# Kernel tuning notes

Measured on AMD Instinct MI355X. Metric: run time of the kernel, lower is better.

The kernel has to match this reference:

```python
import jax, jax.numpy as jnp
import numpy as np

HIDDEN = 3072
INTER = 8192
B, S = 4, 2048


def setup_inputs() -> dict:
    key = jax.random.key(0)
    k1, k2, k3, k4, k5 = jax.random.split(key, 5)
    hidden_states = jax.random.normal(k1, (B, S, HIDDEN), dtype=jnp.float32)
    # int8-valued quantized weights (stored as int32), per-output-channel scales
    gate_up_w_q = jax.random.randint(k2, (2 * INTER, HIDDEN), -128, 128, dtype=jnp.int32)
    gate_up_scale = jax.random.uniform(k3, (2 * INTER,), dtype=jnp.float32) * 0.01
    down_w_q = jax.random.randint(k4, (HIDDEN, INTER), -128, 128, dtype=jnp.int32)
    down_scale = jax.random.uniform(k5, (HIDDEN,), dtype=jnp.float32) * 0.01
    return {
        "hidden_states": hidden_states,
        "gate_up_w_q": gate_up_w_q,
        "gate_up_scale": gate_up_scale,
        "down_w_q": down_w_q,
        "down_scale": down_scale,
    }


def reference(hidden_states, gate_up_w_q, gate_up_scale, down_w_q, down_scale):
    # Inline dequant: W = W_q * scale (per output channel)
    w_gu = gate_up_w_q.astype(jnp.float32) * gate_up_scale[:, None]   # [2I, H]
    up_states = jnp.einsum("bsh,oh->bso", hidden_states, w_gu)        # [B, S, 2I]
    gate, up = jnp.split(up_states, 2, axis=-1)                       # each [B, S, I]
    h = up * jax.nn.silu(gate)                                        # SwiGLU
    w_d = down_w_q.astype(jnp.float32) * down_scale[:, None]          # [H, I]
    return jnp.einsum("bsi,hi->bsh", h, w_d)                          # [B, S, H]
```

## Files before the change

### kernel.cpp

```cpp
#include <hip/hip_runtime.h>
#include <hip/hip_bf16.h>

#define HIDDEN 3072
#define INTER  8192
#define NTOK   8192

typedef __attribute__((ext_vector_type(8))) short bf16x8;
typedef __attribute__((ext_vector_type(4))) float f32x4;

__device__ __forceinline__ void gload_lds16(const void* g, void* l) {
  __builtin_amdgcn_global_load_lds(
      (const __attribute__((address_space(1))) void*)g,
      (__attribute__((address_space(3))) void*)l, 16, 0, 0);
}

__device__ __forceinline__ unsigned short f2bf(float f) {
  unsigned int u = __builtin_bit_cast(unsigned int, f);
  u += 0x7fffu + ((u >> 16) & 1u);
  return (unsigned short)(u >> 16);
}


__global__ void cvt_f32_bf16(const float* __restrict__ in,
                             unsigned short* __restrict__ out, int n4) {
  int i = blockIdx.x * blockDim.x + threadIdx.x;
  if (i >= n4) return;
  float4 v = reinterpret_cast<const float4*>(in)[i];
  ushort4 o;
  o.x = f2bf(v.x); o.y = f2bf(v.y); o.z = f2bf(v.z); o.w = f2bf(v.w);
  reinterpret_cast<ushort4*>(out)[i] = o;
}

__global__ void cvt_i32_bf16(const int* __restrict__ in,
                             unsigned short* __restrict__ out, int n4) {
  int i = blockIdx.x * blockDim.x + threadIdx.x;
  if (i >= n4) return;
  int4 v = reinterpret_cast<const int4*>(in)[i];
  ushort4 o;
  o.x = f2bf((float)v.x); o.y = f2bf((float)v.y);
  o.z = f2bf((float)v.z); o.w = f2bf((float)v.w);
  reinterpret_cast<ushort4*>(out)[i] = o;
}

__global__ void cvt_wgu_perm(const int* __restrict__ in,
                             unsigned short* __restrict__ out) {
  int i4 = blockIdx.x * blockDim.x + threadIdx.x;
  const int RW = HIDDEN / 4;
  if (i4 >= 2 * INTER * RW) return;
  int rowp = i4 / RW;
  int col4 = i4 - rowp * RW;
  int c = ((rowp >> 5) << 4) + (rowp & 15);
  int u = (rowp >> 4) & 1;
  int srow = u * INTER + c;
  int4 v = reinterpret_cast<const int4*>(in)[(size_t)srow * RW + col4];
  ushort4 o;
  o.x = f2bf((float)v.x); o.y = f2bf((float)v.y);
  o.z = f2bf((float)v.z); o.w = f2bf((float)v.w);
  reinterpret_cast<ushort4*>(out)[i4] = o;
}


template<int K, int N, bool SWIGLU>
__global__ __launch_bounds__(512, 2) void gemm8p(
    const unsigned short* __restrict__ A,
    const unsigned short* __restrict__ B,
    const float* __restrict__ scale,
    void* __restrict__ outv)
{
  constexpr int NT = K / 64;
  __shared__ __align__(16) unsigned short lds[2][2][2][256 * 32];

  const int nbn = N / 256;
  const int nwg = (NTOK / 256) * nbn;
  int bid = blockIdx.x;
  int wg = (bid & 7) * (nwg >> 3) + (bid >> 3);
  const int bm = (wg / nbn) * 256;
  const int bn = (wg % nbn) * 256;

  const int tid  = threadIdx.x;
  const int lane = tid & 63;
  const int wid  = tid >> 6;
  const int wr = wid >> 2;
  const int wc = wid & 3;

  const int srow0 = tid >> 2;
  const int srow1 = 128 + (tid >> 2);
  const int scb   = tid & 3;

  const unsigned short* Ab = A + (size_t)bm * K;
  const unsigned short* Bb = B + (size_t)bn * K;

  auto stage = [&](const unsigned short* Gb, int op, int tt, int kh) {
    if (tt >= NT) return;
    int p = tt & 1;
    int kc = tt * 64 + kh * 32;
    unsigned short* lbase = &lds[p][op][kh][0];
    gload_lds16(Gb + (size_t)srow0 * K + kc + ((scb ^ ((srow0 >> 1) & 3)) * 8),
                lbase + (size_t)tid * 8);
    gload_lds16(Gb + (size_t)srow1 * K + kc + ((scb ^ ((srow1 >> 1) & 3)) * 8),
                lbase + (size_t)(512 + tid) * 8);
  };

  auto readA = [&](int p, int kh, int m) -> bf16x8 {
    int row = wr * 128 + m * 16 + (lane & 15);
    int cb = (lane >> 4) ^ ((row >> 1) & 3);
    return *(const bf16x8*)&lds[p][0][kh][row * 32 + cb * 8];
  };
  auto readB = [&](int p, int kh, int n) -> bf16x8 {
    int row = wc * 64 + n * 16 + (lane & 15);
    int cb = (lane >> 4) ^ ((row >> 1) & 3);
    return *(const bf16x8*)&lds[p][1][kh][row * 32 + cb * 8];
  };

  f32x4 acc[8][4] = {};
  bf16x8 af[8];

  stage(Ab, 0, 0, 0);
  stage(Bb, 1, 0, 0);
  stage(Ab, 0, 0, 1);
  stage(Bb, 1, 0, 1);
  stage(Ab, 0, 1, 0);
  stage(Bb, 1, 1, 0);
  stage(Ab, 0, 1, 1);
  asm volatile("s_waitcnt vmcnt(10)" ::: "memory");
  __builtin_amdgcn_s_barrier();

  for (int t = 0; t < NT; ++t) {
    const int pr = t & 1;
#pragma unroll
    for (int m = 0; m < 8; ++m) af[m] = readA(pr, 0, m);
    bf16x8 b0 = readB(pr, 0, 0);
    bf16x8 b1 = readB(pr, 0, 1);
    stage(Bb, 1, t + 1, 1);
    __builtin_amdgcn_s_barrier();
    __builtin_amdgcn_s_setprio(1);
#pragma unroll
    for (int m = 0; m < 8; ++m) {
      acc[m][0] = __builtin_amdgcn_mfma_f32_16x16x32_bf16(af[m], b0, acc[m][0], 0, 0, 0);
      acc[m][1] = __builtin_amdgcn_mfma_f32_16x16x32_bf16(af[m], b1, acc[m][1], 0, 0, 0);
    }
    __builtin_amdgcn_s_setprio(0);
    __builtin_amdgcn_s_barrier();

    b0 = readB(pr, 0, 2);
    b1 = readB(pr, 0, 3);
    stage(Ab, 0, t + 2, 0);
    __builtin_amdgcn_s_barrier();
    __builtin_amdgcn_s_setprio(1);
#pragma unroll
    for (int m = 0; m < 8; ++m) {
      acc[m][2] = __builtin_amdgcn_mfma_f32_16x16x32_bf16(af[m], b0, acc[m][2], 0, 0, 0);
      acc[m][3] = __builtin_amdgcn_mfma_f32_16x16x32_bf16(af[m], b1, acc[m][3], 0, 0, 0);
    }
    __builtin_amdgcn_s_setprio(0);
    if (t + 2 < NT) {
      asm volatile("s_waitcnt vmcnt(10)" ::: "memory");
    } else if (t + 1 < NT) {
      asm volatile("s_waitcnt vmcnt(8)" ::: "memory");
    } else {
      asm volatile("s_waitcnt vmcnt(0)" ::: "memory");
    }
    __builtin_amdgcn_s_barrier();

#pragma unroll
    for (int m = 0; m < 8; ++m) af[m] = readA(pr, 1, m);
    b0 = readB(pr, 1, 0);
    b1 = readB(pr, 1, 1);
    stage(Bb, 1, t + 2, 0);
    __builtin_amdgcn_s_barrier();
    __builtin_amdgcn_s_setprio(1);
#pragma unroll
    for (int m = 0; m < 8; ++m) {
      acc[m][0] = __builtin_amdgcn_mfma_f32_16x16x32_bf16(af[m], b0, acc[m][0], 0, 0, 0);
      acc[m][1] = __builtin_amdgcn_mfma_f32_16x16x32_bf16(af[m], b1, acc[m][1], 0, 0, 0);
    }
    __builtin_amdgcn_s_setprio(0);
    __builtin_amdgcn_s_barrier();

    b0 = readB(pr, 1, 2);
    b1 = readB(pr, 1, 3);
    stage(Ab, 0, t + 2, 1);
    __builtin_amdgcn_s_barrier();
    __builtin_amdgcn_s_setprio(1);
#pragma unroll
    for (int m = 0; m < 8; ++m) {
      acc[m][2] = __builtin_amdgcn_mfma_f32_16x16x32_bf16(af[m], b0, acc[m][2], 0, 0, 0);
      acc[m][3] = __builtin_amdgcn_mfma_f32_16x16x32_bf16(af[m], b1, acc[m][3], 0, 0, 0);
    }
    __builtin_amdgcn_s_setprio(0);
    if (t + 2 < NT) {
      asm volatile("s_waitcnt vmcnt(10)" ::: "memory");
    } else if (t + 1 < NT) {
      asm volatile("s_waitcnt vmcnt(4)" ::: "memory");
    } else {
      asm volatile("s_waitcnt vmcnt(0)" ::: "memory");
    }
    __builtin_amdgcn_s_barrier();
  }

  const int crow0 = (lane >> 4) * 4;
  const int ccol  = lane & 15;
  if constexpr (SWIGLU) {
    unsigned short* H = (unsigned short*)outv;
    const int hbase = (bn >> 1) + wc * 32;
#pragma unroll
    for (int np = 0; np < 2; ++np) {
      int hcol = hbase + np * 16 + ccol;
      float sg = scale[hcol];
      float su = scale[INTER + hcol];
#pragma unroll
      for (int m = 0; m < 8; ++m) {
#pragma unroll
        for (int j = 0; j < 4; ++j) {
          int row = bm + wr * 128 + m * 16 + crow0 + j;
          float g = acc[m][2 * np + 0][j] * sg;
          float u = acc[m][2 * np + 1][j] * su;
          float s = g / (1.0f + __expf(-g));
          H[(size_t)row * INTER + hcol] = f2bf(u * s);
        }
      }
    }
  } else {
    float* O = (float*)outv;
#pragma unroll
    for (int n = 0; n < 4; ++n) {
      int col = bn + wc * 64 + n * 16 + ccol;
      float sc = scale[col];
#pragma unroll
      for (int m = 0; m < 8; ++m) {
#pragma unroll
        for (int j = 0; j < 4; ++j) {
          int row = bm + wr * 128 + m * 16 + crow0 + j;
          O[(size_t)row * N + col] = acc[m][n][j] * sc;
        }
      }
    }
  }
}


extern "C" void kernel_launch(void* const* d_in, const int* in_sizes, int n_in,
                              void* d_out, int out_size, void* d_ws, size_t ws_size,
                              hipStream_t stream) {
  (void)in_sizes; (void)n_in; (void)out_size; (void)ws_size;

  const float* hidden = (const float*)d_in[0];
  const int*   guq    = (const int*)d_in[1];
  const float* gus    = (const float*)d_in[2];
  const int*   dwq    = (const int*)d_in[3];
  const float* dsc    = (const float*)d_in[4];
  float* out = (float*)d_out;

  char* ws = (char*)d_ws;
  unsigned short* xb  = (unsigned short*)(ws);
  unsigned short* wgu = (unsigned short*)(ws + 50331648ull);
  unsigned short* wd  = (unsigned short*)(ws + 150994944ull);
  unsigned short* hb  = (unsigned short*)(ws + 201326592ull);

  {
    int n4 = NTOK * HIDDEN / 4;
    cvt_f32_bf16<<<(n4 + 255) / 256, 256, 0, stream>>>(hidden, xb, n4);
  }
  {
    int n4 = 2 * INTER * HIDDEN / 4;
    cvt_wgu_perm<<<(n4 + 255) / 256, 256, 0, stream>>>(guq, wgu);
  }
  {
    int n4 = HIDDEN * INTER / 4;
    cvt_i32_bf16<<<(n4 + 255) / 256, 256, 0, stream>>>(dwq, wd, n4);
  }

  gemm8p<HIDDEN, 2 * INTER, true>
      <<<(NTOK / 256) * (2 * INTER / 256), 512, 0, stream>>>(xb, wgu, gus, hb);
  gemm8p<INTER, HIDDEN, false>
      <<<(NTOK / 256) * (HIDDEN / 256), 512, 0, stream>>>(hb, wd, dsc, out);
}
```

Before: 1.267 ms.

## Switch to 32x32x16 MFMA tiles and split-K the down GEMM

Both GEMMs move from 16x16x32 to 32x32x16 bf16 MFMA instructions. Per-wave register fragments and LDS reads are reorganised to match, and the gate/up weight permutation now interleaves in 32-row groups so the SwiGLU epilogue still pairs gate and up columns. The down-projection GEMM is split along K into two slices to double the workgroup count and fill the CUs better. Partial results are combined with float atomicAdd into an output that a new kernel zeroes first, which adds extra atomic traffic and makes the summation order nondeterministic.

```diff
diff --git a/kernel.cpp b/kernel.cpp
--- a/kernel.cpp
+++ b/kernel.cpp
@@ -6,7 +6,7 @@
 #define NTOK   8192
 
 typedef __attribute__((ext_vector_type(8))) short bf16x8;
-typedef __attribute__((ext_vector_type(4))) float f32x4;
+typedef __attribute__((ext_vector_type(16))) float f32x16;
 
 __device__ __forceinline__ void gload_lds16(const void* g, void* l) {
   __builtin_amdgcn_global_load_lds(
@@ -49,9 +49,9 @@
   if (i4 >= 2 * INTER * RW) return;
   int rowp = i4 / RW;
   int col4 = i4 - rowp * RW;
-  int c = ((rowp >> 5) << 4) + (rowp & 15);
-  int u = (rowp >> 4) & 1;
-  int srow = u * INTER + c;
+  int h = ((rowp >> 6) << 5) + (rowp & 31);
+  int u = (rowp >> 5) & 1;
+  int srow = u * INTER + h;
   int4 v = reinterpret_cast<const int4*>(in)[(size_t)srow * RW + col4];
   ushort4 o;
   o.x = f2bf((float)v.x); o.y = f2bf((float)v.y);
@@ -59,23 +59,33 @@
   reinterpret_cast<ushort4*>(out)[i4] = o;
 }
 
-
-template<int K, int N, bool SWIGLU>
+__global__ void zero_out(float* __restrict__ out, int n4) {
+  int stride = gridDim.x * blockDim.x;
+  for (int i = blockIdx.x * blockDim.x + threadIdx.x; i < n4; i += stride)
+    reinterpret_cast<float4*>(out)[i] = make_float4(0.f, 0.f, 0.f, 0.f);
+}
+
+
+template<int STRIDE, int KLEN, int N, int KSPLIT, int MODE>
 __global__ __launch_bounds__(512, 2) void gemm8p(
     const unsigned short* __restrict__ A,
     const unsigned short* __restrict__ B,
     const float* __restrict__ scale,
     void* __restrict__ outv)
 {
-  constexpr int NT = K / 64;
+  constexpr int NT = KLEN / 64;
   __shared__ __align__(16) unsigned short lds[2][2][2][256 * 32];
 
   const int nbn = N / 256;
-  const int nwg = (NTOK / 256) * nbn;
+  const int ntmn = (NTOK / 256) * nbn;
+  const int nwg = ntmn * KSPLIT;
   int bid = blockIdx.x;
   int wg = (bid & 7) * (nwg >> 3) + (bid >> 3);
-  const int bm = (wg / nbn) * 256;
-  const int bn = (wg % nbn) * 256;
+  const int kslice = wg / ntmn;
+  const int local = wg - kslice * ntmn;
+  const int bm = (local / nbn) * 256;
+  const int bn = (local % nbn) * 256;
+  const int koff = kslice * KLEN;
 
   const int tid  = threadIdx.x;
   const int lane = tid & 63;
@@ -87,33 +97,34 @@
   const int srow1 = 128 + (tid >> 2);
   const int scb   = tid & 3;
 
-  const unsigned short* Ab = A + (size_t)bm * K;
-  const unsigned short* Bb = B + (size_t)bn * K;
+  const unsigned short* Ab = A + (size_t)bm * STRIDE + koff;
+  const unsigned short* Bb = B + (size_t)bn * STRIDE + koff;
 
   auto stage = [&](const unsigned short* Gb, int op, int tt, int kh) {
     if (tt >= NT) return;
     int p = tt & 1;
     int kc = tt * 64 + kh * 32;
     unsigned short* lbase = &lds[p][op][kh][0];
-    gload_lds16(Gb + (size_t)srow0 * K + kc + ((scb ^ ((srow0 >> 1) & 3)) * 8),
+    gload_lds16(Gb + (size_t)srow0 * STRIDE + kc + ((scb ^ ((srow0 >> 1) & 3)) * 8),
                 lbase + (size_t)tid * 8);
-    gload_lds16(Gb + (size_t)srow1 * K + kc + ((scb ^ ((srow1 >> 1) & 3)) * 8),
+    gload_lds16(Gb + (size_t)srow1 * STRIDE + kc + ((scb ^ ((srow1 >> 1) & 3)) * 8),
                 lbase + (size_t)(512 + tid) * 8);
   };
 
-  auto readA = [&](int p, int kh, int m) -> bf16x8 {
-    int row = wr * 128 + m * 16 + (lane & 15);
-    int cb = (lane >> 4) ^ ((row >> 1) & 3);
+  auto readA = [&](int p, int kh, int m, int ks) -> bf16x8 {
+    int row = wr * 128 + m * 32 + (lane & 31);
+    int cb = (ks * 2 + (lane >> 5)) ^ ((row >> 1) & 3);
     return *(const bf16x8*)&lds[p][0][kh][row * 32 + cb * 8];
   };
-  auto readB = [&](int p, int kh, int n) -> bf16x8 {
-    int row = wc * 64 + n * 16 + (lane & 15);
-    int cb = (lane >> 4) ^ ((row >> 1) & 3);
+  auto readB = [&](int p, int kh, int n, int ks) -> bf16x8 {
+    int row = wc * 64 + n * 32 + (lane & 31);
+    int cb = (ks * 2 + (lane >> 5)) ^ ((row >> 1) & 3);
     return *(const bf16x8*)&lds[p][1][kh][row * 32 + cb * 8];
   };
 
-  f32x4 acc[8][4] = {};
-  bf16x8 af[8];
+  f32x16 acc[4][2] = {};
+  bf16x8 af[4][2];
+  bf16x8 b0, b1;
 
   stage(Ab, 0, 0, 0);
   stage(Bb, 1, 0, 0);
@@ -128,29 +139,32 @@
   for (int t = 0; t < NT; ++t) {
     const int pr = t & 1;
 #pragma unroll
-    for (int m = 0; m < 8; ++m) af[m] = readA(pr, 0, m);
-    bf16x8 b0 = readB(pr, 0, 0);
-    bf16x8 b1 = readB(pr, 0, 1);
+    for (int m = 0; m < 4; ++m) {
+      af[m][0] = readA(pr, 0, m, 0);
+      af[m][1] = readA(pr, 0, m, 1);
+    }
+    b0 = readB(pr, 0, 0, 0);
+    b1 = readB(pr, 0, 0, 1);
     stage(Bb, 1, t + 1, 1);
     __builtin_amdgcn_s_barrier();
     __builtin_amdgcn_s_setprio(1);
 #pragma unroll
-    for (int m = 0; m < 8; ++m) {
-      acc[m][0] = __builtin_amdgcn_mfma_f32_16x16x32_bf16(af[m], b0, acc[m][0], 0, 0, 0);
-      acc[m][1] = __builtin_amdgcn_mfma_f32_16x16x32_bf16(af[m], b1, acc[m][1], 0, 0, 0);
-    }
-    __builtin_amdgcn_s_setprio(0);
-    __builtin_amdgcn_s_barrier();
-
-    b0 = readB(pr, 0, 2);
-    b1 = readB(pr, 0, 3);
+    for (int m = 0; m < 4; ++m) {
+      acc[m][0] = __builtin_amdgcn_mfma_f32_32x32x16_bf16(af[m][0], b0, acc[m][0], 0, 0, 0);
+      acc[m][0] = __builtin_amdgcn_mfma_f32_32x32x16_bf16(af[m][1], b1, acc[m][0], 0, 0, 0);
+    }
+    __builtin_amdgcn_s_setprio(0);
+    __builtin_amdgcn_s_barrier();
+
+    b0 = readB(pr, 0, 1, 0);
+    b1 = readB(pr, 0, 1, 1);
     stage(Ab, 0, t + 2, 0);
     __builtin_amdgcn_s_barrier();
     __builtin_amdgcn_s_setprio(1);
 #pragma unroll
-    for (int m = 0; m < 8; ++m) {
-      acc[m][2] = __builtin_amdgcn_mfma_f32_16x16x32_bf16(af[m], b0, acc[m][2], 0, 0, 0);
-      acc[m][3] = __builtin_amdgcn_mfma_f32_16x16x32_bf16(af[m], b1, acc[m][3], 0, 0, 0);
+    for (int m = 0; m < 4; ++m) {
+      acc[m][1] = __builtin_amdgcn_mfma_f32_32x32x16_bf16(af[m][0], b0, acc[m][1], 0, 0, 0);
+      acc[m][1] = __builtin_amdgcn_mfma_f32_32x32x16_bf16(af[m][1], b1, acc[m][1], 0, 0, 0);
     }
     __builtin_amdgcn_s_setprio(0);
     if (t + 2 < NT) {
@@ -163,29 +177,32 @@
     __builtin_amdgcn_s_barrier();
 
 #pragma unroll
-    for (int m = 0; m < 8; ++m) af[m] = readA(pr, 1, m);
-    b0 = readB(pr, 1, 0);
-    b1 = readB(pr, 1, 1);
+    for (int m = 0; m < 4; ++m) {
+      af[m][0] = readA(pr, 1, m, 0);
+      af[m][1] = readA(pr, 1, m, 1);
+    }
+    b0 = readB(pr, 1, 0, 0);
+    b1 = readB(pr, 1, 0, 1);
     stage(Bb, 1, t + 2, 0);
     __builtin_amdgcn_s_barrier();
     __builtin_amdgcn_s_setprio(1);
 #pragma unroll
-    for (int m = 0; m < 8; ++m) {
-      acc[m][0] = __builtin_amdgcn_mfma_f32_16x16x32_bf16(af[m], b0, acc[m][0], 0, 0, 0);
-      acc[m][1] = __builtin_amdgcn_mfma_f32_16x16x32_bf16(af[m], b1, acc[m][1], 0, 0, 0);
-    }
-    __builtin_amdgcn_s_setprio(0);
-    __builtin_amdgcn_s_barrier();
-
-    b0 = readB(pr, 1, 2);
-    b1 = readB(pr, 1, 3);
+    for (int m = 0; m < 4; ++m) {
+      acc[m][0] = __builtin_amdgcn_mfma_f32_32x32x16_bf16(af[m][0], b0, acc[m][0], 0, 0, 0);
+      acc[m][0] = __builtin_amdgcn_mfma_f32_32x32x16_bf16(af[m][1], b1, acc[m][0], 0, 0, 0);
+    }
+    __builtin_amdgcn_s_setprio(0);
+    __builtin_amdgcn_s_barrier();
+
+    b0 = readB(pr, 1, 1, 0);
+    b1 = readB(pr, 1, 1, 1);
     stage(Ab, 0, t + 2, 1);
     __builtin_amdgcn_s_barrier();
     __builtin_amdgcn_s_setprio(1);
 #pragma unroll
-    for (int m = 0; m < 8; ++m) {
-      acc[m][2] = __builtin_amdgcn_mfma_f32_16x16x32_bf16(af[m], b0, acc[m][2], 0, 0, 0);
-      acc[m][3] = __builtin_amdgcn_mfma_f32_16x16x32_bf16(af[m], b1, acc[m][3], 0, 0, 0);
+    for (int m = 0; m < 4; ++m) {
+      acc[m][1] = __builtin_amdgcn_mfma_f32_32x32x16_bf16(af[m][0], b0, acc[m][1], 0, 0, 0);
+      acc[m][1] = __builtin_amdgcn_mfma_f32_32x32x16_bf16(af[m][1], b1, acc[m][1], 0, 0, 0);
     }
     __builtin_amdgcn_s_setprio(0);
     if (t + 2 < NT) {
@@ -198,40 +215,36 @@
     __builtin_amdgcn_s_barrier();
   }
 
-  const int crow0 = (lane >> 4) * 4;
-  const int ccol  = lane & 15;
-  if constexpr (SWIGLU) {
+  const int ccol  = lane & 31;
+  const int crow4 = 4 * (lane >> 5);
+  if constexpr (MODE == 1) {
     unsigned short* H = (unsigned short*)outv;
-    const int hbase = (bn >> 1) + wc * 32;
-#pragma unroll
-    for (int np = 0; np < 2; ++np) {
-      int hcol = hbase + np * 16 + ccol;
-      float sg = scale[hcol];
-      float su = scale[INTER + hcol];
-#pragma unroll
-      for (int m = 0; m < 8; ++m) {
-#pragma unroll
-        for (int j = 0; j < 4; ++j) {
-          int row = bm + wr * 128 + m * 16 + crow0 + j;
-          float g = acc[m][2 * np + 0][j] * sg;
-          float u = acc[m][2 * np + 1][j] * su;
-          float s = g / (1.0f + __expf(-g));
-          H[(size_t)row * INTER + hcol] = f2bf(u * s);
-        }
+    const int hcol = (bn >> 1) + wc * 32 + ccol;
+    const float sg = scale[hcol];
+    const float su = scale[INTER + hcol];
+#pragma unroll
+    for (int m = 0; m < 4; ++m) {
+#pragma unroll
+      for (int r = 0; r < 16; ++r) {
+        int row = bm + wr * 128 + m * 32 + (r & 3) + 8 * (r >> 2) + crow4;
+        float g = acc[m][0][r] * sg;
+        float u = acc[m][1][r] * su;
+        float s = g / (1.0f + __expf(-g));
+        H[(size_t)row * INTER + hcol] = f2bf(u * s);
       }
     }
   } else {
     float* O = (float*)outv;
 #pragma unroll
-    for (int n = 0; n < 4; ++n) {
-      int col = bn + wc * 64 + n * 16 + ccol;
+    for (int n = 0; n < 2; ++n) {
+      int col = bn + wc * 64 + n * 32 + ccol;
       float sc = scale[col];
 #pragma unroll
-      for (int m = 0; m < 8; ++m) {
-#pragma unroll
-        for (int j = 0; j < 4; ++j) {
-          int row = bm + wr * 128 + m * 16 + crow0 + j;
-          O[(size_t)row * N + col] = acc[m][n][j] * sc;
+      for (int m = 0; m < 4; ++m) {
+#pragma unroll
+        for (int r = 0; r < 16; ++r) {
+          int row = bm + wr * 128 + m * 32 + (r & 3) + 8 * (r >> 2) + crow4;
+          atomicAdd(&O[(size_t)row * N + col], acc[m][n][r] * sc);
         }
       }
     }
@@ -269,9 +282,10 @@
     int n4 = HIDDEN * INTER / 4;
     cvt_i32_bf16<<<(n4 + 255) / 256, 256, 0, stream>>>(dwq, wd, n4);
   }
-
-  gemm8p<HIDDEN, 2 * INTER, true>
+  zero_out<<<2048, 256, 0, stream>>>(out, NTOK * HIDDEN / 4);
+
+  gemm8p<HIDDEN, HIDDEN, 2 * INTER, 1, 1>
       <<<(NTOK / 256) * (2 * INTER / 256), 512, 0, stream>>>(xb, wgu, gus, hb);
-  gemm8p<INTER, HIDDEN, false>
-      <<<(NTOK / 256) * (HIDDEN / 256), 512, 0, stream>>>(hb, wd, dsc, out);
-}
+  gemm8p<INTER, INTER / 2, HIDDEN, 2, 2>
+      <<<(NTOK / 256) * (HIDDEN / 256) * 2, 512, 0, stream>>>(hb, wd, dsc, out);
+}
```

After: 1.428 ms. 12.7% more time.
